# Kernel tuning notes

Hardware: AMD Instinct MI355X
Metric: run time of the kernel (lower is better)

## Reference

```python
import jax, jax.numpy as jnp
import numpy as np

B, L, C, H = 4, 1024, 768, 12
D = C // H  # head_ch = 64


def setup_inputs() -> dict:
    key = jax.random.key(0)
    ks = jax.random.split(key, 8)
    s = 1.0 / np.sqrt(C)
    return {
        "inputs_q": jax.random.normal(ks[0], (B, L, C), jnp.float32),
        "inputs_kv": jax.random.normal(ks[1], (B, L, C), jnp.float32),
        "Wq": jax.random.normal(ks[2], (C, H * D), jnp.float32) * s,
        "Wk": jax.random.normal(ks[3], (C, H * D), jnp.float32) * s,
        "Wv": jax.random.normal(ks[4], (C, H * D), jnp.float32) * s,
        "Wout": jax.random.normal(ks[5], (H * D, C), jnp.float32) * s,
        "W_pre": jax.random.normal(ks[6], (H, H), jnp.float32) * (1.0 / np.sqrt(H)),
        "W_post": jax.random.normal(ks[7], (H, H), jnp.float32) * (1.0 / np.sqrt(H)),
    }


def reference(inputs_q, inputs_kv, Wq, Wk, Wv, Wout, W_pre, W_post):
    # Linear projections (no bias), split into heads: b l (h d) -> b h l d
    def split_heads(x):
        b, l, _ = x.shape
        return x.reshape(b, l, H, D).transpose(0, 2, 1, 3)

    q = split_heads(inputs_q @ Wq) / jnp.sqrt(jnp.asarray(D, inputs_q.dtype))
    k = split_heads(inputs_kv @ Wk)
    v = split_heads(inputs_kv @ Wv)

    # Attention logits [b, h, l, k]
    weights = jnp.einsum('bhld,bhkd->bhlk', q, k)
    # Talking-heads: learned cross-head mixing pre-softmax
    weights = jnp.einsum('bhlk,hi->bilk', weights, W_pre)
    weights = jax.nn.softmax(weights, axis=-1)
    # Talking-heads post-softmax mixing
    weights = jnp.einsum('bhlk,hi->bilk', weights, W_post)

    scores = jnp.einsum('bhlk,bhkd->bhld', weights, v)
    scores = scores.transpose(0, 2, 1, 3).reshape(B, L, H * D)  # b l (h d)
    return scores @ Wout
```

## Files before the change

kernel.cpp:

```cpp
#include <hip/hip_runtime.h>
#include <hip/hip_bf16.h>

#define BB 4
#define LL 1024
#define CC 768
#define HH 12
#define DD 64

typedef unsigned short ushort_t;
typedef __attribute__((ext_vector_type(8))) short bf16x8;
typedef __attribute__((ext_vector_type(4))) float f32x4;
typedef __attribute__((ext_vector_type(2))) float f32x2;
typedef __attribute__((ext_vector_type(2))) unsigned u32x2;

__device__ inline ushort_t f2bf(float x) {
    union { float f; unsigned u; } v; v.f = x;
    unsigned r = (v.u + 0x7FFFu + ((v.u >> 16) & 1u)) >> 16;
    return (ushort_t)r;
}
__device__ inline float u2f(unsigned u) {
    union { unsigned u; float f; } v; v.u = u;
    return v.f;
}
__device__ inline unsigned pack2bf(float lo, float hi) {
    union { __hip_bfloat162 v; unsigned u; } r;
    r.v = __float22bfloat162_rn(make_float2(lo, hi));
    return r.u;
}

__device__ inline void stage_rows(const ushort_t* __restrict__ g, int stride,
                                  ushort_t* lds, int nbytes, int wave, int lane) {
    const int ko = (lane & 3) << 3;
    const int rsub = lane >> 2;
    for (int off = wave * 1024; off < nbytes; off += 4096) {
        int row = (off >> 6) + rsub;
        __builtin_amdgcn_global_load_lds(
            (const __attribute__((address_space(1))) void*)(g + (size_t)row * stride + ko),
            (__attribute__((address_space(3))) void*)(lds + (off >> 1)),
            16, 0, 0);
    }
}

__global__ __launch_bounds__(256) void prep(const float* __restrict__ q, const float* __restrict__ kv,
                                            const float* __restrict__ w0, const float* __restrict__ w1,
                                            const float* __restrict__ w2, const float* __restrict__ w3,
                                            ushort_t* __restrict__ qo, ushort_t* __restrict__ kvo,
                                            ushort_t* __restrict__ o0, ushort_t* __restrict__ o1,
                                            ushort_t* __restrict__ o2, ushort_t* __restrict__ o3,
                                            float* __restrict__ Zp) {
    __shared__ float t[32][33];
    const int bx = blockIdx.x;
    if (bx < 3072) {
        const float* src = bx < 1536 ? q : kv;
        ushort_t* dst = bx < 1536 ? qo : kvo;
        int bb = bx < 1536 ? bx : bx - 1536;
        size_t i = ((size_t)bb * 256 + threadIdx.x) * 8;
        float4 a = *(const float4*)(src + i);
        float4 b = *(const float4*)(src + i + 4);
        ushort_t u[8] = {f2bf(a.x), f2bf(a.y), f2bf(a.z), f2bf(a.w),
                         f2bf(b.x), f2bf(b.y), f2bf(b.z), f2bf(b.w)};
        *(uint4*)(dst + i) = *(uint4*)u;
    } else if (bx < 5376) {
        int w = bx - 3072;
        int z = w / 576, rem = w % 576;
        const float* W = z == 0 ? w0 : z == 1 ? w1 : z == 2 ? w2 : w3;
        ushort_t* Wt   = z == 0 ? o0 : z == 1 ? o1 : z == 2 ? o2 : o3;
        const int c = threadIdx.x & 31, r0 = threadIdx.x >> 5;
        const int kb = (rem / 24) * 32, nb = (rem % 24) * 32;
#pragma unroll
        for (int i = 0; i < 4; ++i)
            t[r0 + 8 * i][c] = W[(size_t)(kb + r0 + 8 * i) * CC + nb + c];
        __syncthreads();
#pragma unroll
        for (int i = 0; i < 4; ++i)
            Wt[(size_t)(nb + r0 + 8 * i) * CC + kb + c] = f2bf(t[c][r0 + 8 * i]);
    } else {
        Zp[(bx - 5376) * 256 + threadIdx.x] = 0.f;
    }
}

__global__ __launch_bounds__(256) void proj_gemm(const ushort_t* __restrict__ Aq,
                                                 const ushort_t* __restrict__ Akv,
                                                 const ushort_t* __restrict__ Wqt,
                                                 const ushort_t* __restrict__ Wkt,
                                                 const ushort_t* __restrict__ Wvt,
                                                 ushort_t* __restrict__ Qo,
                                                 ushort_t* __restrict__ Ko,
                                                 ushort_t* __restrict__ Vto) {
    const int z = blockIdx.z;
    const ushort_t* A  = (z == 0) ? Aq : Akv;
    const ushort_t* Wt = (z == 0) ? Wqt : (z == 1 ? Wkt : Wvt);

    __shared__ __align__(16) ushort_t a_lds[128 * 32];
    __shared__ __align__(16) ushort_t b_lds[128 * 32];

    const int tid = threadIdx.x;
    const int bm = blockIdx.x * 128, bn = blockIdx.y * 128;
    const int wave = tid >> 6, lane = tid & 63;
    const int quad = lane >> 4, lq = lane & 15;
    const int wr = wave >> 1, wc = wave & 1;

    f32x4 acc[4][4] = {};

    for (int k0 = 0; k0 < CC; k0 += 32) {
        stage_rows(A + (size_t)bm * CC + k0, CC, a_lds, 8192, wave, lane);
        stage_rows(Wt + (size_t)bn * CC + k0, CC, b_lds, 8192, wave, lane);
        __syncthreads();
        bf16x8 af[4], bfr[4];
#pragma unroll
        for (int mi = 0; mi < 4; ++mi)
            af[mi] = *(bf16x8*)&a_lds[(wr * 64 + mi * 16 + lq) * 32 + quad * 8];
#pragma unroll
        for (int ni = 0; ni < 4; ++ni)
            bfr[ni] = *(bf16x8*)&b_lds[(wc * 64 + ni * 16 + lq) * 32 + quad * 8];
#pragma unroll
        for (int mi = 0; mi < 4; ++mi)
#pragma unroll
            for (int ni = 0; ni < 4; ++ni)
                acc[mi][ni] = __builtin_amdgcn_mfma_f32_16x16x32_bf16(af[mi], bfr[ni], acc[mi][ni], 0, 0, 0);
        __syncthreads();
    }

    const float scale = (z == 0) ? 0.125f : 1.0f;
#pragma unroll
    for (int mi = 0; mi < 4; ++mi)
#pragma unroll
        for (int ni = 0; ni < 4; ++ni)
#pragma unroll
            for (int r = 0; r < 4; ++r) {
                int row = bm + wr * 64 + mi * 16 + quad * 4 + r;
                int col = bn + wc * 64 + ni * 16 + lq;
                int b = row >> 10, l = row & 1023, h = col >> 6, d = col & 63;
                ushort_t v = f2bf(acc[mi][ni][r] * scale);
                if (z == 2) {
                    Vto[((size_t)(b * HH + h) * DD + d) * LL + l] = v;
                } else {
                    size_t off = (size_t)(b * HH + h) * (LL * DD)
                               + (size_t)(((l >> 4) * 8 + (d >> 3)) * 128 + (l & 15) * 8 + (d & 7));
                    if (z == 0) Qo[off] = v;
                    else        Ko[off] = v;
                }
            }
}

__global__ __launch_bounds__(256) void qk_premix(const ushort_t* __restrict__ Qf,
                                                 const ushort_t* __restrict__ Kf,
                                                 const float* __restrict__ Wpre,
                                                 ushort_t* __restrict__ E,
                                                 float* __restrict__ Z) {
    const int tid = threadIdx.x;
    const int lane = tid & 63, wave = tid >> 6;
    const int quad = lane >> 4, lq = lane & 15;
    const int wr = wave >> 1, wc = wave & 1;

    const int x = blockIdx.x;
    const int xcd = x & 7;
    const int b = xcd >> 1;
    const int s = x >> 3;
    const int bk = (s & 31) << 5;
    const int bl = ((((s >> 5) << 1) | (xcd & 1))) << 5;

    const ushort_t* Kp = Kf + (size_t)b * HH * LL * DD
                       + (size_t)(((bk >> 4) + wr) * 1024 + quad * 128 + lq * 8);
    const ushort_t* Qp = Qf + (size_t)b * HH * LL * DD
                       + (size_t)(((bl >> 4) + wc) * 1024 + quad * 128 + lq * 8);

    f32x4 acc[HH] = {};
#pragma unroll
    for (int h = 0; h < HH; ++h) {
        const size_t ho = (size_t)h * (LL * DD);
        bf16x8 ka0 = *(const bf16x8*)(Kp + ho);
        bf16x8 ka1 = *(const bf16x8*)(Kp + ho + 512);
        bf16x8 qb0 = *(const bf16x8*)(Qp + ho);
        bf16x8 qb1 = *(const bf16x8*)(Qp + ho + 512);
        acc[h] = __builtin_amdgcn_mfma_f32_16x16x32_bf16(ka0, qb0, acc[h], 0, 0, 0);
        acc[h] = __builtin_amdgcn_mfma_f32_16x16x32_bf16(ka1, qb1, acc[h], 0, 0, 0);
    }

    unsigned pk[6][4];
#pragma unroll
    for (int i2 = 0; i2 < 6; ++i2) {
        f32x4 m0 = {}, m1 = {};
#pragma unroll
        for (int h = 0; h < HH; ++h) {
            m0 += acc[h] * Wpre[h * HH + 2 * i2];
            m1 += acc[h] * Wpre[h * HH + 2 * i2 + 1];
        }
#pragma unroll
        for (int r = 0; r < 4; ++r)
            pk[i2][r] = pack2bf(__expf(m0[r]), __expf(m1[r]));
    }

    float zp[HH];
#pragma unroll
    for (int i2 = 0; i2 < 6; ++i2) {
        float s0 = 0.f, s1 = 0.f;
#pragma unroll
        for (int r = 0; r < 4; ++r) {
            s0 += u2f(pk[i2][r] << 16);
            s1 += u2f(pk[i2][r] & 0xFFFF0000u);
        }
        zp[2 * i2] = s0; zp[2 * i2 + 1] = s1;
    }
#pragma unroll
    for (int i = 0; i < HH; ++i) {
        zp[i] += __shfl_xor(zp[i], 16);
        zp[i] += __shfl_xor(zp[i], 32);
    }
    if (quad == 0) {
#pragma unroll
        for (int i = 0; i < HH; ++i)
            atomicAdd(&Z[((size_t)b * HH + i) * LL + bl + wc * 16 + lq], zp[i]);
    }

#pragma unroll
    for (int r = 0; r < 4; ++r) {
        ushort_t* ep = E + (((size_t)b * LL + bk + wr * 16 + quad * 4 + r) * LL
                            + bl + wc * 16 + lq) * HH;
        u32x2 s0; s0.x = pk[0][r]; s0.y = pk[1][r];
        u32x2 s1; s1.x = pk[2][r]; s1.y = pk[3][r];
        u32x2 s2; s2.x = pk[4][r]; s2.y = pk[5][r];
        __builtin_nontemporal_store(s0, (u32x2*)ep);
        __builtin_nontemporal_store(s1, (u32x2*)(ep + 4));
        __builtin_nontemporal_store(s2, (u32x2*)(ep + 8));
    }
}

__global__ __launch_bounds__(512) void pv_postmix(const ushort_t* __restrict__ E,
                                                  const ushort_t* __restrict__ Vt,
                                                  const float* __restrict__ Wpost,
                                                  const float* __restrict__ Z,
                                                  ushort_t* __restrict__ att) {
    __shared__ __align__(16) ushort_t v_lds[HH * 64 * 64];
    __shared__ __align__(16) ushort_t p_lds[HH * 16 * 64];

    const int tid = threadIdx.x;
    const int bl = blockIdx.x * 16;
    const int b  = blockIdx.y;
    const int lane = tid & 63, wave = tid >> 6;
    const int quad = lane >> 4, lq = lane & 15;
    const int ig = (wave >> 2) * 6;
    const int wd = wave & 3;
    const int lmix = tid & 15, kp = tid >> 4;

    float invZ[HH];
#pragma unroll
    for (int h = 0; h < HH; ++h)
        invZ[h] = 1.0f / Z[((size_t)b * HH + h) * LL + bl + lmix];

    f32x4 acc[6] = {};

#pragma unroll 1
    for (int kt = 0; kt < 16; ++kt) {
#pragma unroll
        for (int j = 0; j < 12; ++j) {
            const int o = (tid << 4) + (j << 13);
            const int row = o >> 7;
            const int cs = ((o >> 4) & 7) ^ (row & 7);
            const ushort_t* src = Vt + ((size_t)b * HH * 64 + row) * LL + kt * 64 + cs * 8;
            __builtin_amdgcn_global_load_lds(
                (const __attribute__((address_space(1))) void*)src,
                (__attribute__((address_space(3))) void*)(v_lds + (o >> 1)), 16, 0, 0);
        }

        const int kg = kt * 64 + kp * 2;
        const ushort_t* ep = E + (((size_t)b * LL + kg) * LL + bl + lmix) * HH;
        u32x2 ua = __builtin_nontemporal_load((const u32x2*)ep);
        u32x2 ub = __builtin_nontemporal_load((const u32x2*)(ep + 4));
        u32x2 uc = __builtin_nontemporal_load((const u32x2*)(ep + 8));
        u32x2 va = __builtin_nontemporal_load((const u32x2*)(ep + (size_t)LL * HH));
        u32x2 vb = __builtin_nontemporal_load((const u32x2*)(ep + (size_t)LL * HH + 4));
        u32x2 vc = __builtin_nontemporal_load((const u32x2*)(ep + (size_t)LL * HH + 8));
        unsigned w0[6] = {ua.x, ua.y, ub.x, ub.y, uc.x, uc.y};
        unsigned w1[6] = {va.x, va.y, vb.x, vb.y, vc.x, vc.y};

        f32x2 m[HH] = {};
#pragma unroll
        for (int h2 = 0; h2 < 6; ++h2) {
            f32x2 pe, po;
            pe.x = u2f(w0[h2] << 16);           pe.y = u2f(w1[h2] << 16);
            po.x = u2f(w0[h2] & 0xFFFF0000u);   po.y = u2f(w1[h2] & 0xFFFF0000u);
            pe *= invZ[2 * h2];
            po *= invZ[2 * h2 + 1];
#pragma unroll
            for (int i = 0; i < HH; ++i) {
                m[i] += pe * Wpost[(2 * h2) * HH + i];
                m[i] += po * Wpost[(2 * h2 + 1) * HH + i];
            }
        }
        {
            const int cs = (kp >> 2) ^ (lmix & 7);
            unsigned* pw = (unsigned*)p_lds;
#pragma unroll
            for (int i = 0; i < HH; ++i)
                pw[(i * 16 + lmix) * 32 + cs * 4 + (kp & 3)] = pack2bf(m[i].x, m[i].y);
        }
        __syncthreads();

#pragma unroll
        for (int k0 = 0; k0 < 2; ++k0)
#pragma unroll
            for (int ii = 0; ii < 6; ++ii) {
                const int hh = ig + ii;
                const int ch = ((k0 << 2) + quad) ^ (lq & 7);
                bf16x8 pa  = *(bf16x8*)&p_lds[(hh * 16 + lq) * 64 + ch * 8];
                bf16x8 vbf = *(bf16x8*)&v_lds[(hh * 64 + wd * 16 + lq) * 64 + ch * 8];
                acc[ii] = __builtin_amdgcn_mfma_f32_16x16x32_bf16(pa, vbf, acc[ii], 0, 0, 0);
            }
        __syncthreads();
    }

#pragma unroll
    for (int ii = 0; ii < 6; ++ii)
#pragma unroll
        for (int r = 0; r < 4; ++r)
            att[((size_t)b * LL + bl + quad * 4 + r) * CC + (ig + ii) * 64 + wd * 16 + lq] =
                f2bf(acc[ii][r]);
}

__global__ __launch_bounds__(256) void out_gemm(const ushort_t* __restrict__ A,
                                                const ushort_t* __restrict__ Wt,
                                                float* __restrict__ out) {
    __shared__ __align__(16) ushort_t a_lds[128 * 32];
    __shared__ __align__(16) ushort_t b_lds[64 * 32];

    const int tid = threadIdx.x;
    const int bm = blockIdx.x * 128, bn = blockIdx.y * 64;
    const int wave = tid >> 6, lane = tid & 63;
    const int quad = lane >> 4, lq = lane & 15;
    const int wr = wave >> 1, wc = wave & 1;

    f32x4 acc[4][2] = {};

    for (int k0 = 0; k0 < CC; k0 += 32) {
        stage_rows(A + (size_t)bm * CC + k0, CC, a_lds, 8192, wave, lane);
        stage_rows(Wt + (size_t)bn * CC + k0, CC, b_lds, 4096, wave, lane);
        __syncthreads();
        bf16x8 af[4], bfr[2];
#pragma unroll
        for (int mi = 0; mi < 4; ++mi)
            af[mi] = *(bf16x8*)&a_lds[(wr * 64 + mi * 16 + lq) * 32 + quad * 8];
#pragma unroll
        for (int ni = 0; ni < 2; ++ni)
            bfr[ni] = *(bf16x8*)&b_lds[(wc * 32 + ni * 16 + lq) * 32 + quad * 8];
#pragma unroll
        for (int mi = 0; mi < 4; ++mi)
#pragma unroll
            for (int ni = 0; ni < 2; ++ni)
                acc[mi][ni] = __builtin_amdgcn_mfma_f32_16x16x32_bf16(af[mi], bfr[ni], acc[mi][ni], 0, 0, 0);
        __syncthreads();
    }

#pragma unroll
    for (int mi = 0; mi < 4; ++mi)
#pragma unroll
        for (int ni = 0; ni < 2; ++ni)
#pragma unroll
            for (int r = 0; r < 4; ++r) {
                int row = bm + wr * 64 + mi * 16 + quad * 4 + r;
                int col = bn + wc * 32 + ni * 16 + lq;
                out[(size_t)row * CC + col] = acc[mi][ni][r];
            }
}

extern "C" void kernel_launch(void* const* d_in, const int* in_sizes, int n_in,
                              void* d_out, int out_size, void* d_ws, size_t ws_size,
                              hipStream_t stream) {
    const float* inputs_q  = (const float*)d_in[0];
    const float* inputs_kv = (const float*)d_in[1];
    const float* Wq   = (const float*)d_in[2];
    const float* Wk   = (const float*)d_in[3];
    const float* Wv   = (const float*)d_in[4];
    const float* Wout = (const float*)d_in[5];
    const float* Wpre  = (const float*)d_in[6];
    const float* Wpost = (const float*)d_in[7];
    float* out = (float*)d_out;

    const size_t nS   = (size_t)BB * HH * LL * LL;
    const size_t nQKV = (size_t)BB * HH * LL * DD;
    const size_t nW   = (size_t)CC * CC;

    ushort_t* Eb   = (ushort_t*)d_ws;
    ushort_t* Qb   = Eb + nS;
    ushort_t* Kb   = Qb + nQKV;
    ushort_t* Vtb  = Kb + nQKV;
    ushort_t* attb = Vtb + nQKV;
    ushort_t* inq  = attb + nQKV;
    ushort_t* inkv = inq + nQKV;
    ushort_t* Wqt  = inkv + nQKV;
    ushort_t* Wkt  = Wqt + nW;
    ushort_t* Wvt  = Wkt + nW;
    ushort_t* Wot  = Wvt + nW;
    float*    Zb   = (float*)(Wot + nW);

    dim3 blk(256);

    prep<<<dim3(5568), blk, 0, stream>>>(inputs_q, inputs_kv, Wq, Wk, Wv, Wout,
                                         inq, inkv, Wqt, Wkt, Wvt, Wot, Zb);
    proj_gemm<<<dim3(32, 6, 3), blk, 0, stream>>>(inq, inkv, Wqt, Wkt, Wvt, Qb, Kb, Vtb);
    qk_premix<<<dim3(4096), blk, 0, stream>>>(Qb, Kb, Wpre, Eb, Zb);
    pv_postmix<<<dim3(LL / 16, BB), dim3(512), 0, stream>>>(Eb, Vtb, Wpost, Zb, attb);
    out_gemm<<<dim3(32, 12), blk, 0, stream>>>(attb, Wot, out);
}
```

Measured before the change: 251.8 us.

## Restructure pv_postmix: direct V loads, double-buffered P, E prefetch, XCD mapping

The V tile is no longer staged through LDS; each wave loads its MFMA B-operand straight from global memory. P is double-buffered in LDS, so only one barrier per iteration is needed. The next E chunk is prefetched into registers while the current one is mixed. Blocks are remapped on a flat grid so each batch's blocks share an XCD for L2 locality. Direct V reads rely on cache hits and may raise global traffic and register pressure.

```diff
diff --git a/kernel.cpp b/kernel.cpp
--- a/kernel.cpp
+++ b/kernel.cpp
@@ -231,49 +231,42 @@
                                                   const float* __restrict__ Wpost,
                                                   const float* __restrict__ Z,
                                                   ushort_t* __restrict__ att) {
-    __shared__ __align__(16) ushort_t v_lds[HH * 64 * 64];
-    __shared__ __align__(16) ushort_t p_lds[HH * 16 * 64];
+    __shared__ __align__(16) ushort_t p_lds[2][HH * 16 * 64];
 
     const int tid = threadIdx.x;
-    const int bl = blockIdx.x * 16;
-    const int b  = blockIdx.y;
     const int lane = tid & 63, wave = tid >> 6;
     const int quad = lane >> 4, lq = lane & 15;
     const int ig = (wave >> 2) * 6;
     const int wd = wave & 3;
     const int lmix = tid & 15, kp = tid >> 4;
 
+    const int bid = blockIdx.x;
+    const int xcd = bid & 7;
+    const int b = xcd >> 1;
+    const int bl = ((((bid >> 3) << 1) | (xcd & 1))) << 4;
+
     float invZ[HH];
 #pragma unroll
     for (int h = 0; h < HH; ++h)
         invZ[h] = 1.0f / Z[((size_t)b * HH + h) * LL + bl + lmix];
 
+    const size_t vrow = ((size_t)(b * HH) * DD + wd * 16 + lq) * LL;
+    const ushort_t* ebase = E + (((size_t)b * LL + kp * 2) * LL + bl + lmix) * HH;
+    const size_t estep = (size_t)LL * HH;
+
     f32x4 acc[6] = {};
+    u32x2 er[6];
+
+#pragma unroll
+    for (int j = 0; j < 3; ++j) {
+        er[j]     = __builtin_nontemporal_load((const u32x2*)(ebase + 4 * j));
+        er[j + 3] = __builtin_nontemporal_load((const u32x2*)(ebase + estep + 4 * j));
+    }
 
 #pragma unroll 1
     for (int kt = 0; kt < 16; ++kt) {
-#pragma unroll
-        for (int j = 0; j < 12; ++j) {
-            const int o = (tid << 4) + (j << 13);
-            const int row = o >> 7;
-            const int cs = ((o >> 4) & 7) ^ (row & 7);
-            const ushort_t* src = Vt + ((size_t)b * HH * 64 + row) * LL + kt * 64 + cs * 8;
-            __builtin_amdgcn_global_load_lds(
-                (const __attribute__((address_space(1))) void*)src,
-                (__attribute__((address_space(3))) void*)(v_lds + (o >> 1)), 16, 0, 0);
-        }
-
-        const int kg = kt * 64 + kp * 2;
-        const ushort_t* ep = E + (((size_t)b * LL + kg) * LL + bl + lmix) * HH;
-        u32x2 ua = __builtin_nontemporal_load((const u32x2*)ep);
-        u32x2 ub = __builtin_nontemporal_load((const u32x2*)(ep + 4));
-        u32x2 uc = __builtin_nontemporal_load((const u32x2*)(ep + 8));
-        u32x2 va = __builtin_nontemporal_load((const u32x2*)(ep + (size_t)LL * HH));
-        u32x2 vb = __builtin_nontemporal_load((const u32x2*)(ep + (size_t)LL * HH + 4));
-        u32x2 vc = __builtin_nontemporal_load((const u32x2*)(ep + (size_t)LL * HH + 8));
-        unsigned w0[6] = {ua.x, ua.y, ub.x, ub.y, uc.x, uc.y};
-        unsigned w1[6] = {va.x, va.y, vb.x, vb.y, vc.x, vc.y};
-
+        unsigned w0[6] = {er[0].x, er[0].y, er[1].x, er[1].y, er[2].x, er[2].y};
+        unsigned w1[6] = {er[3].x, er[3].y, er[4].x, er[4].y, er[5].x, er[5].y};
         f32x2 m[HH] = {};
 #pragma unroll
         for (int h2 = 0; h2 < 6; ++h2) {
@@ -288,26 +281,41 @@
                 m[i] += po * Wpost[(2 * h2 + 1) * HH + i];
             }
         }
+
+        if (kt < 15) {
+            const ushort_t* ep = ebase + (size_t)(kt + 1) * 64 * estep;
+#pragma unroll
+            for (int j = 0; j < 3; ++j) {
+                er[j]     = __builtin_nontemporal_load((const u32x2*)(ep + 4 * j));
+                er[j + 3] = __builtin_nontemporal_load((const u32x2*)(ep + estep + 4 * j));
+            }
+        }
+
         {
             const int cs = (kp >> 2) ^ (lmix & 7);
-            unsigned* pw = (unsigned*)p_lds;
+            unsigned* pw = (unsigned*)p_lds[kt & 1];
 #pragma unroll
             for (int i = 0; i < HH; ++i)
                 pw[(i * 16 + lmix) * 32 + cs * 4 + (kp & 3)] = pack2bf(m[i].x, m[i].y);
         }
-        __syncthreads();
-
+
+        asm volatile("s_waitcnt lgkmcnt(0)" ::: "memory");
+        __builtin_amdgcn_s_barrier();
+        asm volatile("" ::: "memory");
+
+        const ushort_t* pb = p_lds[kt & 1];
 #pragma unroll
         for (int k0 = 0; k0 < 2; ++k0)
 #pragma unroll
             for (int ii = 0; ii < 6; ++ii) {
                 const int hh = ig + ii;
-                const int ch = ((k0 << 2) + quad) ^ (lq & 7);
-                bf16x8 pa  = *(bf16x8*)&p_lds[(hh * 16 + lq) * 64 + ch * 8];
-                bf16x8 vbf = *(bf16x8*)&v_lds[(hh * 64 + wd * 16 + lq) * 64 + ch * 8];
+                const int chl = (k0 << 2) + quad;
+                const int chs = chl ^ (lq & 7);
+                bf16x8 pa  = *(bf16x8*)&pb[(hh * 16 + lq) * 64 + chs * 8];
+                bf16x8 vbf = *(const bf16x8*)(Vt + vrow + (size_t)hh * (DD * LL)
+                                              + kt * 64 + chl * 8);
                 acc[ii] = __builtin_amdgcn_mfma_f32_16x16x32_bf16(pa, vbf, acc[ii], 0, 0, 0);
             }
-        __syncthreads();
     }
 
 #pragma unroll
@@ -399,6 +407,6 @@
                                          inq, inkv, Wqt, Wkt, Wvt, Wot, Zb);
     proj_gemm<<<dim3(32, 6, 3), blk, 0, stream>>>(inq, inkv, Wqt, Wkt, Wvt, Qb, Kb, Vtb);
     qk_premix<<<dim3(4096), blk, 0, stream>>>(Qb, Kb, Wpre, Eb, Zb);
-    pv_postmix<<<dim3(LL / 16, BB), dim3(512), 0, stream>>>(Eb, Vtb, Wpost, Zb, attb);
+    pv_postmix<<<dim3(256), dim3(512), 0, stream>>>(Eb, Vtb, Wpost, Zb, attb);
     out_gemm<<<dim3(32, 12), blk, 0, stream>>>(attb, Wot, out);
 }
```

Result: slower. 265.3 us (+5.4%).
